# Kernel tuning notes

Hardware: AMD Instinct MI355X
Metric: run time of the kernel (lower is better)

The kernel has to match this reference:

```python
import jax, jax.numpy as jnp
import numpy as np

T, D, O, E, R = 16384, 4096, 4096, 8, 64  # tokens, in_feat, out_feat, n_adapters, max_rank


def setup_inputs() -> dict:
    key = jax.random.key(0)
    ks = jax.random.split(key, 6)
    x = jax.random.normal(ks[0], (T, D), jnp.float32)
    base_output = jax.random.normal(ks[1], (T, O), jnp.float32)
    A = jax.random.normal(ks[2], (E, D, R), jnp.float32) * 0.02  # loraA per adapter
    B = jax.random.normal(ks[3], (E, R, O), jnp.float32) * 0.02  # loraB per adapter
    scaling = jax.random.uniform(ks[4], (E,), jnp.float32, 0.5, 2.0)  # lora_alpha/rank per adapter
    adapter_ids = jax.random.randint(ks[5], (T,), 0, E, dtype=jnp.int32)  # per-token routing
    return {"x": x, "base_output": base_output, "A": A, "B": B,
            "scaling": scaling, "adapter_ids": adapter_ids}


def reference(x, base_output, A, B, scaling, adapter_ids):
    """S-LoRA batched multi-adapter forward: out = base + (x @ A_i) @ B_i * s_i,
    with adapter i routed per token. Expressed as E masked low-rank GEMMs
    (loop over the small fixed adapter set, vectorized over tokens)."""
    out = base_output
    for e in range(E):
        gate = (adapter_ids == e).astype(x.dtype) * scaling[e]  # (T,)
        h = x @ A[e]                                            # (T, R)
        out = out + (h @ B[e]) * gate[:, None]                  # (T, O)
    return out
```

## Files before the change

kernel.cpp:

```cpp
#include <hip/hip_runtime.h>

#define TT 16384
#define DD 4096
#define OO 4096
#define NE 8
#define RRK 64
#define KSPLIT 4
#define KCHUNK 1024

typedef _Float16 f16x8 __attribute__((ext_vector_type(8)));
typedef float f32x4 __attribute__((ext_vector_type(4)));

#define CNT_OFF 0
#define PERM_OFF 1024
#define AT_OFF (1u << 20)
#define BT_OFF (5u << 20)
#define HP_OFF (9u << 20)

__global__ void prep_kernel(const int* __restrict__ ids,
                            const float* __restrict__ A,
                            const float* __restrict__ B,
                            int* __restrict__ cnt,
                            int* __restrict__ perm,
                            _Float16* __restrict__ At,
                            _Float16* __restrict__ Bt) {
  const int bid = blockIdx.x, tid = threadIdx.x;
  if (bid < 64) {
    int t = bid * 256 + tid;
    int e = ids[t];
    int pos = atomicAdd(&cnt[e], 1);
    perm[e * TT + pos] = t;
    return;
  }
  __shared__ float tile[64][65];
  if (bid < 576) {
    int idx = bid - 64;
    int e = idx >> 6, kb = (idx & 63) << 6;
    #pragma unroll
    for (int i = 0; i < 16; ++i) {
      int lin = i * 256 + tid;
      int kr = lin >> 6, r = lin & 63;
      tile[kr][r] = A[((size_t)e * DD + kb + kr) * RRK + r];
    }
    __syncthreads();
    #pragma unroll
    for (int i = 0; i < 16; ++i) {
      int lin = i * 256 + tid;
      int r = lin >> 6, kk = lin & 63;
      At[((size_t)e * RRK + r) * DD + kb + kk] = (_Float16)tile[kk][r];
    }
  } else {
    int idx = bid - 576;
    int e = idx >> 6, ob = (idx & 63) << 6;
    #pragma unroll
    for (int i = 0; i < 16; ++i) {
      int lin = i * 256 + tid;
      int r = lin >> 6, o = lin & 63;
      tile[r][o] = B[((size_t)e * RRK + r) * OO + ob + o];
    }
    __syncthreads();
    #pragma unroll
    for (int i = 0; i < 16; ++i) {
      int lin = i * 256 + tid;
      int o = lin >> 6, r2 = lin & 63;
      Bt[((size_t)e * OO + ob + o) * RRK + r2] = (_Float16)tile[r2][o];
    }
  }
}

__global__ __launch_bounds__(256, 2)
void lora_stage1(const float* __restrict__ x,
                 const _Float16* __restrict__ At,
                 const int* __restrict__ cnt,
                 const int* __restrict__ perm,
                 _Float16* __restrict__ HP) {
  __shared__ _Float16 Xs[64][72];
  __shared__ _Float16 As[64][72];
  __shared__ int toks[64];
  const int tid = threadIdx.x;
  const int lane = tid & 63, w = tid >> 6;

  int tiles = 0;
  #pragma unroll
  for (int ee = 0; ee < NE; ++ee) tiles += (cnt[ee] + 63) >> 6;

  for (int wi = blockIdx.x; wi < tiles * KSPLIT; wi += gridDim.x) {
    int tile = wi >> 2, s = wi & 3;
    int e = 0, base = 0, n_e = 0;
    {
      int acc0 = 0;
      #pragma unroll
      for (int ee = 0; ee < NE; ++ee) {
        int c = cnt[ee];
        int tl = (c + 63) >> 6;
        if (tile >= acc0 && tile < acc0 + tl) { e = ee; base = acc0; n_e = c; }
        acc0 += tl;
      }
    }
    int m0 = (tile - base) << 6;
    int kbase = s * KCHUNK;

    if (tid < 64) {
      int rloc = m0 + tid;
      toks[tid] = (rloc < n_e) ? perm[e * TT + rloc] : -1;
    }
    __syncthreads();

    const int srow = tid >> 2;
    const int seg = (tid & 3) << 4;
    int tk0 = toks[srow];
    if (tk0 < 0) tk0 = toks[0];
    const float* xp = x + (size_t)tk0 * DD + seg;
    const _Float16* ap = At + ((size_t)e * RRK + srow) * DD + seg;

    f32x4 acc[4] = {};

    for (int k0 = kbase; k0 < kbase + KCHUNK; k0 += 64) {
      float4 v0 = *(const float4*)(xp + k0);
      float4 v1 = *(const float4*)(xp + k0 + 4);
      float4 v2 = *(const float4*)(xp + k0 + 8);
      float4 v3 = *(const float4*)(xp + k0 + 12);
      f16x8 xa, xb;
      xa[0] = (_Float16)v0.x; xa[1] = (_Float16)v0.y;
      xa[2] = (_Float16)v0.z; xa[3] = (_Float16)v0.w;
      xa[4] = (_Float16)v1.x; xa[5] = (_Float16)v1.y;
      xa[6] = (_Float16)v1.z; xa[7] = (_Float16)v1.w;
      xb[0] = (_Float16)v2.x; xb[1] = (_Float16)v2.y;
      xb[2] = (_Float16)v2.z; xb[3] = (_Float16)v2.w;
      xb[4] = (_Float16)v3.x; xb[5] = (_Float16)v3.y;
      xb[6] = (_Float16)v3.z; xb[7] = (_Float16)v3.w;
      *(f16x8*)&Xs[srow][seg] = xa;
      *(f16x8*)&Xs[srow][seg + 8] = xb;
      *(f16x8*)&As[srow][seg] = *(const f16x8*)(ap + k0);
      *(f16x8*)&As[srow][seg + 8] = *(const f16x8*)(ap + k0 + 8);
      __syncthreads();

      const int mr = w * 16 + (lane & 15);
      const int kq = (lane >> 4) << 3;
      #pragma unroll
      for (int ks = 0; ks < 2; ++ks) {
        f16x8 af = *(const f16x8*)&Xs[mr][ks * 32 + kq];
        #pragma unroll
        for (int nf = 0; nf < 4; ++nf) {
          f16x8 bfr = *(const f16x8*)&As[nf * 16 + (lane & 15)][ks * 32 + kq];
          acc[nf] = __builtin_amdgcn_mfma_f32_16x16x32_f16(af, bfr, acc[nf], 0, 0, 0);
        }
      }
      __syncthreads();
    }

    const int rq = (lane >> 4) << 2;
    #pragma unroll
    for (int rg = 0; rg < 4; ++rg) {
      int tk = toks[w * 16 + rq + rg];
      if (tk >= 0) {
        _Float16* hp = HP + ((size_t)s * TT + tk) * RRK + (lane & 15);
        #pragma unroll
        for (int nf = 0; nf < 4; ++nf) {
          hp[nf * 16] = (_Float16)acc[nf][rg];
        }
      }
    }
    __syncthreads();
  }
}

__global__ __launch_bounds__(256, 2)
void lora_stage2(const float* __restrict__ baseo,
                 const _Float16* __restrict__ Bt,
                 const _Float16* __restrict__ HP,
                 const float* __restrict__ scaling,
                 const int* __restrict__ cnt,
                 const int* __restrict__ perm,
                 float* __restrict__ out) {
  __shared__ _Float16 Hs[64][72];
  __shared__ _Float16 Bs[256][72];
  __shared__ int toks[64];
  const int tid = threadIdx.x;
  const int lane = tid & 63, w = tid >> 6;

  int tot = 0;
  #pragma unroll
  for (int ee = 0; ee < NE; ++ee) tot += ((cnt[ee] + 63) >> 6) << 4;

  for (int wi = blockIdx.x; wi < tot; wi += gridDim.x) {
    int e = 0, base = 0, n_e = 0;
    {
      int acc0 = 0;
      #pragma unroll
      for (int ee = 0; ee < NE; ++ee) {
        int c = cnt[ee];
        int tl = ((c + 63) >> 6) << 4;
        if (wi >= acc0 && wi < acc0 + tl) { e = ee; base = acc0; n_e = c; }
        acc0 += tl;
      }
    }
    int local = wi - base;
    int tiles_m = (n_e + 63) >> 6;
    int mt = local % tiles_m;
    int nt = local / tiles_m;
    int m0 = mt << 6, o0 = nt << 8;

    if (tid < 64) {
      int rloc = m0 + tid;
      toks[tid] = (rloc < n_e) ? perm[e * TT + rloc] : -1;
    }
    __syncthreads();

    {
      const f16x8* bp = (const f16x8*)(Bt + ((size_t)e * OO + o0 + tid) * RRK);
      #pragma unroll
      for (int j = 0; j < 8; ++j) *(f16x8*)&Bs[tid][j * 8] = bp[j];
    }
    {
      float s_e = scaling[e];
      int srow = tid >> 2, seg = (tid & 3) << 4;
      int tk = toks[srow];
      if (tk < 0) tk = toks[0];
      float sum[16];
      #pragma unroll
      for (int i = 0; i < 16; ++i) sum[i] = 0.f;
      #pragma unroll
      for (int s = 0; s < KSPLIT; ++s) {
        const f16x8* hp = (const f16x8*)(HP + ((size_t)s * TT + tk) * RRK + seg);
        f16x8 h0 = hp[0], h1 = hp[1];
        #pragma unroll
        for (int i = 0; i < 8; ++i) { sum[i] += (float)h0[i]; sum[8 + i] += (float)h1[i]; }
      }
      f16x8 o0v, o1v;
      #pragma unroll
      for (int i = 0; i < 8; ++i) { o0v[i] = (_Float16)(sum[i] * s_e); o1v[i] = (_Float16)(sum[8 + i] * s_e); }
      *(f16x8*)&Hs[srow][seg] = o0v;
      *(f16x8*)&Hs[srow][seg + 8] = o1v;
    }
    __syncthreads();

    f32x4 acc[16] = {};
    const int kq = (lane >> 4) << 3;
    const int lr = lane & 15;
    #pragma unroll
    for (int ks = 0; ks < 2; ++ks) {
      f16x8 hf = *(const f16x8*)&Hs[w * 16 + lr][ks * 32 + kq];
      #pragma unroll
      for (int of = 0; of < 16; ++of) {
        f16x8 bfr = *(const f16x8*)&Bs[of * 16 + lr][ks * 32 + kq];
        acc[of] = __builtin_amdgcn_mfma_f32_16x16x32_f16(bfr, hf, acc[of], 0, 0, 0);
      }
    }

    int tk = toks[w * 16 + lr];
    if (tk >= 0) {
      const int g4 = (lane >> 4) << 2;
      size_t rowoff = (size_t)tk * OO + o0 + g4;
      #pragma unroll
      for (int of = 0; of < 16; ++of) {
        size_t off = rowoff + of * 16;
        float4 b4 = *(const float4*)(baseo + off);
        float4 r4;
        r4.x = b4.x + acc[of][0];
        r4.y = b4.y + acc[of][1];
        r4.z = b4.z + acc[of][2];
        r4.w = b4.w + acc[of][3];
        *(float4*)(out + off) = r4;
      }
    }
    __syncthreads();
  }
}

extern "C" void kernel_launch(void* const* d_in, const int* in_sizes, int n_in,
                              void* d_out, int out_size, void* d_ws, size_t ws_size,
                              hipStream_t stream) {
  const float* x = (const float*)d_in[0];
  const float* baseo = (const float*)d_in[1];
  const float* A = (const float*)d_in[2];
  const float* B = (const float*)d_in[3];
  const float* scaling = (const float*)d_in[4];
  const int* ids = (const int*)d_in[5];
  float* out = (float*)d_out;
  char* ws = (char*)d_ws;

  int* cnt = (int*)(ws + CNT_OFF);
  int* perm = (int*)(ws + PERM_OFF);
  _Float16* At = (_Float16*)(ws + AT_OFF);
  _Float16* Bt = (_Float16*)(ws + BT_OFF);
  _Float16* HP = (_Float16*)(ws + HP_OFF);

  hipMemsetAsync(cnt, 0, NE * sizeof(int), stream);
  hipLaunchKernelGGL(prep_kernel, dim3(1088), dim3(256), 0, stream,
                     ids, A, B, cnt, perm, At, Bt);
  hipLaunchKernelGGL(lora_stage1, dim3(1056), dim3(256), 0, stream,
                     x, At, cnt, perm, HP);
  hipLaunchKernelGGL(lora_stage2, dim3(4208), dim3(256), 0, stream,
                     baseo, Bt, HP, scaling, cnt, perm, out);
}
```

Baseline: 300.4 us.

## Drop shared-memory staging, double K-split, add separate split-K reduce kernel

```diff
diff --git a/kernel.cpp b/kernel.cpp
--- a/kernel.cpp
+++ b/kernel.cpp
@@ -5,10 +5,11 @@
 #define OO 4096
 #define NE 8
 #define RRK 64
-#define KSPLIT 4
-#define KCHUNK 1024
+#define KSPLIT 8
+#define KCHUNK 512
 
 typedef _Float16 f16x8 __attribute__((ext_vector_type(8)));
+typedef _Float16 f16x4 __attribute__((ext_vector_type(4)));
 typedef float f32x4 __attribute__((ext_vector_type(4)));
 
 #define CNT_OFF 0
@@ -16,6 +17,7 @@
 #define AT_OFF (1u << 20)
 #define BT_OFF (5u << 20)
 #define HP_OFF (9u << 20)
+#define H_OFF (41u << 20)
 
 __global__ void prep_kernel(const int* __restrict__ ids,
                             const float* __restrict__ A,
@@ -68,24 +70,23 @@
   }
 }
 
-__global__ __launch_bounds__(256, 2)
+__global__ __launch_bounds__(256, 4)
 void lora_stage1(const float* __restrict__ x,
                  const _Float16* __restrict__ At,
                  const int* __restrict__ cnt,
                  const int* __restrict__ perm,
-                 _Float16* __restrict__ HP) {
-  __shared__ _Float16 Xs[64][72];
-  __shared__ _Float16 As[64][72];
-  __shared__ int toks[64];
+                 float* __restrict__ HP) {
   const int tid = threadIdx.x;
   const int lane = tid & 63, w = tid >> 6;
+  const int lr = lane & 15;
+  const int kq = (lane >> 4) << 3;
 
   int tiles = 0;
   #pragma unroll
   for (int ee = 0; ee < NE; ++ee) tiles += (cnt[ee] + 63) >> 6;
 
   for (int wi = blockIdx.x; wi < tiles * KSPLIT; wi += gridDim.x) {
-    int tile = wi >> 2, s = wi & 3;
+    int tile = wi >> 3, s = wi & 7;
     int e = 0, base = 0, n_e = 0;
     {
       int acc0 = 0;
@@ -100,84 +101,81 @@
     int m0 = (tile - base) << 6;
     int kbase = s * KCHUNK;
 
-    if (tid < 64) {
-      int rloc = m0 + tid;
-      toks[tid] = (rloc < n_e) ? perm[e * TT + rloc] : -1;
-    }
-    __syncthreads();
-
-    const int srow = tid >> 2;
-    const int seg = (tid & 3) << 4;
-    int tk0 = toks[srow];
-    if (tk0 < 0) tk0 = toks[0];
-    const float* xp = x + (size_t)tk0 * DD + seg;
-    const _Float16* ap = At + ((size_t)e * RRK + srow) * DD + seg;
+    int arow = m0 + w * 16 + lr;
+    int atok = perm[e * TT + (arow < n_e ? arow : n_e - 1)];
+    const float* xp = x + (size_t)atok * DD + kbase + kq;
+    const _Float16* ap = At + (size_t)e * RRK * DD + kbase + kq;
 
     f32x4 acc[4] = {};
 
-    for (int k0 = kbase; k0 < kbase + KCHUNK; k0 += 64) {
-      float4 v0 = *(const float4*)(xp + k0);
-      float4 v1 = *(const float4*)(xp + k0 + 4);
-      float4 v2 = *(const float4*)(xp + k0 + 8);
-      float4 v3 = *(const float4*)(xp + k0 + 12);
-      f16x8 xa, xb;
-      xa[0] = (_Float16)v0.x; xa[1] = (_Float16)v0.y;
-      xa[2] = (_Float16)v0.z; xa[3] = (_Float16)v0.w;
-      xa[4] = (_Float16)v1.x; xa[5] = (_Float16)v1.y;
-      xa[6] = (_Float16)v1.z; xa[7] = (_Float16)v1.w;
-      xb[0] = (_Float16)v2.x; xb[1] = (_Float16)v2.y;
-      xb[2] = (_Float16)v2.z; xb[3] = (_Float16)v2.w;
-      xb[4] = (_Float16)v3.x; xb[5] = (_Float16)v3.y;
-      xb[6] = (_Float16)v3.z; xb[7] = (_Float16)v3.w;
-      *(f16x8*)&Xs[srow][seg] = xa;
-      *(f16x8*)&Xs[srow][seg + 8] = xb;
-      *(f16x8*)&As[srow][seg] = *(const f16x8*)(ap + k0);
-      *(f16x8*)&As[srow][seg + 8] = *(const f16x8*)(ap + k0 + 8);
-      __syncthreads();
-
-      const int mr = w * 16 + (lane & 15);
-      const int kq = (lane >> 4) << 3;
+    for (int k0 = 0; k0 < KCHUNK; k0 += 64) {
+      f16x8 xa[2];
       #pragma unroll
       for (int ks = 0; ks < 2; ++ks) {
-        f16x8 af = *(const f16x8*)&Xs[mr][ks * 32 + kq];
+        float4 u0 = *(const float4*)(xp + k0 + ks * 32);
+        float4 u1 = *(const float4*)(xp + k0 + ks * 32 + 4);
+        f16x8 v;
+        v[0] = (_Float16)u0.x; v[1] = (_Float16)u0.y;
+        v[2] = (_Float16)u0.z; v[3] = (_Float16)u0.w;
+        v[4] = (_Float16)u1.x; v[5] = (_Float16)u1.y;
+        v[6] = (_Float16)u1.z; v[7] = (_Float16)u1.w;
+        xa[ks] = v;
+      }
+      #pragma unroll
+      for (int ks = 0; ks < 2; ++ks) {
         #pragma unroll
         for (int nf = 0; nf < 4; ++nf) {
-          f16x8 bfr = *(const f16x8*)&As[nf * 16 + (lane & 15)][ks * 32 + kq];
-          acc[nf] = __builtin_amdgcn_mfma_f32_16x16x32_f16(af, bfr, acc[nf], 0, 0, 0);
+          f16x8 bfr = *(const f16x8*)(ap + (size_t)(nf * 16 + lr) * DD + k0 + ks * 32);
+          acc[nf] = __builtin_amdgcn_mfma_f32_16x16x32_f16(xa[ks], bfr, acc[nf], 0, 0, 0);
         }
       }
-      __syncthreads();
     }
 
     const int rq = (lane >> 4) << 2;
     #pragma unroll
     for (int rg = 0; rg < 4; ++rg) {
-      int tk = toks[w * 16 + rq + rg];
-      if (tk >= 0) {
-        _Float16* hp = HP + ((size_t)s * TT + tk) * RRK + (lane & 15);
+      int row = m0 + w * 16 + rq + rg;
+      if (row < n_e) {
+        int tk = perm[e * TT + row];
+        float* hp = HP + ((size_t)s * TT + tk) * RRK + lr;
         #pragma unroll
-        for (int nf = 0; nf < 4; ++nf) {
-          hp[nf * 16] = (_Float16)acc[nf][rg];
-        }
-      }
-    }
-    __syncthreads();
-  }
-}
-
-__global__ __launch_bounds__(256, 2)
+        for (int nf = 0; nf < 4; ++nf) hp[nf * 16] = acc[nf][rg];
+      }
+    }
+  }
+}
+
+__global__ void lora_reduce(const float* __restrict__ HP,
+                            const float* __restrict__ scaling,
+                            const int* __restrict__ ids,
+                            _Float16* __restrict__ H) {
+  int i = blockIdx.x * 256 + threadIdx.x;
+  int t = i >> 4;
+  int rg = (i & 15) << 2;
+  float s = scaling[ids[t]];
+  f32x4 sum = {};
+  #pragma unroll
+  for (int sp = 0; sp < KSPLIT; ++sp) {
+    sum += *(const f32x4*)(HP + ((size_t)sp * TT + t) * RRK + rg);
+  }
+  f16x4 h;
+  #pragma unroll
+  for (int j = 0; j < 4; ++j) h[j] = (_Float16)(sum[j] * s);
+  *(f16x4*)(H + (size_t)t * RRK + rg) = h;
+}
+
+__global__ __launch_bounds__(256, 4)
 void lora_stage2(const float* __restrict__ baseo,
                  const _Float16* __restrict__ Bt,
-                 const _Float16* __restrict__ HP,
-                 const float* __restrict__ scaling,
+                 const _Float16* __restrict__ H,
                  const int* __restrict__ cnt,
                  const int* __restrict__ perm,
                  float* __restrict__ out) {
-  __shared__ _Float16 Hs[64][72];
-  __shared__ _Float16 Bs[256][72];
-  __shared__ int toks[64];
   const int tid = threadIdx.x;
   const int lane = tid & 63, w = tid >> 6;
+  const int lr = lane & 15;
+  const int kq = (lane >> 4) << 3;
+  const int g4 = (lane >> 4) << 2;
 
   int tot = 0;
   #pragma unroll
@@ -201,56 +199,29 @@
     int nt = local / tiles_m;
     int m0 = mt << 6, o0 = nt << 8;
 
-    if (tid < 64) {
-      int rloc = m0 + tid;
-      toks[tid] = (rloc < n_e) ? perm[e * TT + rloc] : -1;
-    }
-    __syncthreads();
-
-    {
-      const f16x8* bp = (const f16x8*)(Bt + ((size_t)e * OO + o0 + tid) * RRK);
-      #pragma unroll
-      for (int j = 0; j < 8; ++j) *(f16x8*)&Bs[tid][j * 8] = bp[j];
-    }
-    {
-      float s_e = scaling[e];
-      int srow = tid >> 2, seg = (tid & 3) << 4;
-      int tk = toks[srow];
-      if (tk < 0) tk = toks[0];
-      float sum[16];
-      #pragma unroll
-      for (int i = 0; i < 16; ++i) sum[i] = 0.f;
-      #pragma unroll
-      for (int s = 0; s < KSPLIT; ++s) {
-        const f16x8* hp = (const f16x8*)(HP + ((size_t)s * TT + tk) * RRK + seg);
-        f16x8 h0 = hp[0], h1 = hp[1];
-        #pragma unroll
-        for (int i = 0; i < 8; ++i) { sum[i] += (float)h0[i]; sum[8 + i] += (float)h1[i]; }
-      }
-      f16x8 o0v, o1v;
-      #pragma unroll
-      for (int i = 0; i < 8; ++i) { o0v[i] = (_Float16)(sum[i] * s_e); o1v[i] = (_Float16)(sum[8 + i] * s_e); }
-      *(f16x8*)&Hs[srow][seg] = o0v;
-      *(f16x8*)&Hs[srow][seg + 8] = o1v;
-    }
-    __syncthreads();
-
-    f32x4 acc[16] = {};
-    const int kq = (lane >> 4) << 3;
-    const int lr = lane & 15;
-    #pragma unroll
-    for (int ks = 0; ks < 2; ++ks) {
-      f16x8 hf = *(const f16x8*)&Hs[w * 16 + lr][ks * 32 + kq];
-      #pragma unroll
-      for (int of = 0; of < 16; ++of) {
-        f16x8 bfr = *(const f16x8*)&Bs[of * 16 + lr][ks * 32 + kq];
-        acc[of] = __builtin_amdgcn_mfma_f32_16x16x32_f16(bfr, hf, acc[of], 0, 0, 0);
-      }
-    }
-
-    int tk = toks[w * 16 + lr];
-    if (tk >= 0) {
-      const int g4 = (lane >> 4) << 2;
+    int row = m0 + w * 16 + lr;
+    bool valid = row < n_e;
+    int tk = perm[e * TT + (valid ? row : n_e - 1)];
+
+    const _Float16* hp = H + (size_t)tk * RRK + kq;
+    f16x8 hf0 = *(const f16x8*)(hp);
+    f16x8 hf1 = *(const f16x8*)(hp + 32);
+
+    const _Float16* bp = Bt + ((size_t)e * OO + o0 + lr) * RRK + kq;
+
+    f32x4 acc[16];
+    #pragma unroll
+    for (int of = 0; of < 16; ++of) acc[of] = (f32x4){0.f, 0.f, 0.f, 0.f};
+
+    #pragma unroll
+    for (int of = 0; of < 16; ++of) {
+      f16x8 b0 = *(const f16x8*)(bp + (size_t)of * 16 * RRK);
+      f16x8 b1 = *(const f16x8*)(bp + (size_t)of * 16 * RRK + 32);
+      acc[of] = __builtin_amdgcn_mfma_f32_16x16x32_f16(b0, hf0, acc[of], 0, 0, 0);
+      acc[of] = __builtin_amdgcn_mfma_f32_16x16x32_f16(b1, hf1, acc[of], 0, 0, 0);
+    }
+
+    if (valid) {
       size_t rowoff = (size_t)tk * OO + o0 + g4;
       #pragma unroll
       for (int of = 0; of < 16; ++of) {
@@ -264,7 +235,6 @@
         *(float4*)(out + off) = r4;
       }
     }
-    __syncthreads();
   }
 }
 
@@ -284,13 +254,16 @@
   int* perm = (int*)(ws + PERM_OFF);
   _Float16* At = (_Float16*)(ws + AT_OFF);
   _Float16* Bt = (_Float16*)(ws + BT_OFF);
-  _Float16* HP = (_Float16*)(ws + HP_OFF);
+  float* HP = (float*)(ws + HP_OFF);
+  _Float16* H = (_Float16*)(ws + H_OFF);
 
   hipMemsetAsync(cnt, 0, NE * sizeof(int), stream);
   hipLaunchKernelGGL(prep_kernel, dim3(1088), dim3(256), 0, stream,
                      ids, A, B, cnt, perm, At, Bt);
-  hipLaunchKernelGGL(lora_stage1, dim3(1056), dim3(256), 0, stream,
+  hipLaunchKernelGGL(lora_stage1, dim3(2048), dim3(256), 0, stream,
                      x, At, cnt, perm, HP);
-  hipLaunchKernelGGL(lora_stage2, dim3(4208), dim3(256), 0, stream,
-                     baseo, Bt, HP, scaling, cnt, perm, out);
-}
+  hipLaunchKernelGGL(lora_reduce, dim3(1024), dim3(256), 0, stream,
+                     HP, scaling, ids, H);
+  hipLaunchKernelGGL(lora_stage2, dim3(4096), dim3(256), 0, stream,
+                     baseo, Bt, H, cnt, perm, out);
+}
```

Result: slower. 349.8 us (+16.5%).

## Split-K reduction into own kernel; keep B fragments in registers across tiles

Applied to the files above, without the earlier changes.

```diff
diff --git a/kernel.cpp b/kernel.cpp
--- a/kernel.cpp
+++ b/kernel.cpp
@@ -9,6 +9,7 @@
 #define KCHUNK 1024
 
 typedef _Float16 f16x8 __attribute__((ext_vector_type(8)));
+typedef _Float16 f16x4 __attribute__((ext_vector_type(4)));
 typedef float f32x4 __attribute__((ext_vector_type(4)));
 
 #define CNT_OFF 0
@@ -16,6 +17,7 @@
 #define AT_OFF (1u << 20)
 #define BT_OFF (5u << 20)
 #define HP_OFF (9u << 20)
+#define H_OFF (18u << 20)
 
 __global__ void prep_kernel(const int* __restrict__ ids,
                             const float* __restrict__ A,
@@ -165,23 +167,46 @@
   }
 }
 
+__global__ void lora_reduce(const _Float16* __restrict__ HP,
+                            const float* __restrict__ scaling,
+                            const int* __restrict__ ids,
+                            _Float16* __restrict__ H) {
+  int i = blockIdx.x * 256 + threadIdx.x;
+  int t = i >> 4;
+  int rg = (i & 15) << 2;
+  float s = scaling[ids[t]];
+  float sum[4] = {0.f, 0.f, 0.f, 0.f};
+  #pragma unroll
+  for (int sp = 0; sp < KSPLIT; ++sp) {
+    f16x4 h = *(const f16x4*)(HP + ((size_t)sp * TT + t) * RRK + rg);
+    #pragma unroll
+    for (int j = 0; j < 4; ++j) sum[j] += (float)h[j];
+  }
+  f16x4 hv;
+  #pragma unroll
+  for (int j = 0; j < 4; ++j) hv[j] = (_Float16)(sum[j] * s);
+  *(f16x4*)(H + (size_t)t * RRK + rg) = hv;
+}
+
 __global__ __launch_bounds__(256, 2)
 void lora_stage2(const float* __restrict__ baseo,
                  const _Float16* __restrict__ Bt,
-                 const _Float16* __restrict__ HP,
-                 const float* __restrict__ scaling,
+                 const _Float16* __restrict__ H,
                  const int* __restrict__ cnt,
                  const int* __restrict__ perm,
                  float* __restrict__ out) {
-  __shared__ _Float16 Hs[64][72];
-  __shared__ _Float16 Bs[256][72];
-  __shared__ int toks[64];
   const int tid = threadIdx.x;
   const int lane = tid & 63, w = tid >> 6;
+  const int lr = lane & 15;
+  const int kq = (lane >> 4) << 3;
+  const int g4 = (lane >> 4) << 2;
 
   int tot = 0;
   #pragma unroll
-  for (int ee = 0; ee < NE; ++ee) tot += ((cnt[ee] + 63) >> 6) << 4;
+  for (int ee = 0; ee < NE; ++ee) {
+    int tl = (cnt[ee] + 63) >> 6;
+    tot += ((tl + 3) >> 2) << 4;
+  }
 
   for (int wi = blockIdx.x; wi < tot; wi += gridDim.x) {
     int e = 0, base = 0, n_e = 0;
@@ -190,81 +215,73 @@
       #pragma unroll
       for (int ee = 0; ee < NE; ++ee) {
         int c = cnt[ee];
-        int tl = ((c + 63) >> 6) << 4;
-        if (wi >= acc0 && wi < acc0 + tl) { e = ee; base = acc0; n_e = c; }
-        acc0 += tl;
+        int work = ((((c + 63) >> 6) + 3) >> 2) << 4;
+        if (wi >= acc0 && wi < acc0 + work) { e = ee; base = acc0; n_e = c; }
+        acc0 += work;
       }
     }
     int local = wi - base;
+    int panel = local & 15;
+    int ch = local >> 4;
+    int o0 = panel << 8;
+    int tbase = ch << 2;
     int tiles_m = (n_e + 63) >> 6;
-    int mt = local % tiles_m;
-    int nt = local / tiles_m;
-    int m0 = mt << 6, o0 = nt << 8;
-
-    if (tid < 64) {
-      int rloc = m0 + tid;
-      toks[tid] = (rloc < n_e) ? perm[e * TT + rloc] : -1;
-    }
-    __syncthreads();
-
+    int ntile = tiles_m - tbase;
+    if (ntile > 4) ntile = 4;
+
+    f16x8 bf0[16], bf1[16];
     {
-      const f16x8* bp = (const f16x8*)(Bt + ((size_t)e * OO + o0 + tid) * RRK);
-      #pragma unroll
-      for (int j = 0; j < 8; ++j) *(f16x8*)&Bs[tid][j * 8] = bp[j];
-    }
-    {
-      float s_e = scaling[e];
-      int srow = tid >> 2, seg = (tid & 3) << 4;
-      int tk = toks[srow];
-      if (tk < 0) tk = toks[0];
-      float sum[16];
-      #pragma unroll
-      for (int i = 0; i < 16; ++i) sum[i] = 0.f;
-      #pragma unroll
-      for (int s = 0; s < KSPLIT; ++s) {
-        const f16x8* hp = (const f16x8*)(HP + ((size_t)s * TT + tk) * RRK + seg);
-        f16x8 h0 = hp[0], h1 = hp[1];
+      const _Float16* bp = Bt + ((size_t)e * OO + o0 + lr) * RRK + kq;
+      #pragma unroll
+      for (int of = 0; of < 16; ++of) {
+        bf0[of] = *(const f16x8*)(bp + (size_t)of * 16 * RRK);
+        bf1[of] = *(const f16x8*)(bp + (size_t)of * 16 * RRK + 32);
+      }
+    }
+
+    const int prow = e * TT;
+    int row_c = tbase * 64 + w * 16 + lr;
+    bool v_c = row_c < n_e;
+    int tk_c = perm[prow + (v_c ? row_c : n_e - 1)];
+    f16x8 hf0_c = *(const f16x8*)(H + (size_t)tk_c * RRK + kq);
+    f16x8 hf1_c = *(const f16x8*)(H + (size_t)tk_c * RRK + kq + 32);
+
+    for (int m = 0; m < ntile; ++m) {
+      int row_n = row_c + 64;
+      bool v_n = false; int tk_n = tk_c;
+      f16x8 hf0_n = hf0_c, hf1_n = hf1_c;
+      if (m + 1 < ntile) {
+        v_n = row_n < n_e;
+        tk_n = perm[prow + (v_n ? row_n : n_e - 1)];
+        hf0_n = *(const f16x8*)(H + (size_t)tk_n * RRK + kq);
+        hf1_n = *(const f16x8*)(H + (size_t)tk_n * RRK + kq + 32);
+      }
+
+      f32x4 acc[16];
+      #pragma unroll
+      for (int of = 0; of < 16; ++of) acc[of] = (f32x4){0.f, 0.f, 0.f, 0.f};
+      #pragma unroll
+      for (int of = 0; of < 16; ++of) {
+        acc[of] = __builtin_amdgcn_mfma_f32_16x16x32_f16(bf0[of], hf0_c, acc[of], 0, 0, 0);
+        acc[of] = __builtin_amdgcn_mfma_f32_16x16x32_f16(bf1[of], hf1_c, acc[of], 0, 0, 0);
+      }
+
+      if (v_c) {
+        size_t rowoff = (size_t)tk_c * OO + o0 + g4;
         #pragma unroll
-        for (int i = 0; i < 8; ++i) { sum[i] += (float)h0[i]; sum[8 + i] += (float)h1[i]; }
-      }
-      f16x8 o0v, o1v;
-      #pragma unroll
-      for (int i = 0; i < 8; ++i) { o0v[i] = (_Float16)(sum[i] * s_e); o1v[i] = (_Float16)(sum[8 + i] * s_e); }
-      *(f16x8*)&Hs[srow][seg] = o0v;
-      *(f16x8*)&Hs[srow][seg + 8] = o1v;
-    }
-    __syncthreads();
-
-    f32x4 acc[16] = {};
-    const int kq = (lane >> 4) << 3;
-    const int lr = lane & 15;
-    #pragma unroll
-    for (int ks = 0; ks < 2; ++ks) {
-      f16x8 hf = *(const f16x8*)&Hs[w * 16 + lr][ks * 32 + kq];
-      #pragma unroll
-      for (int of = 0; of < 16; ++of) {
-        f16x8 bfr = *(const f16x8*)&Bs[of * 16 + lr][ks * 32 + kq];
-        acc[of] = __builtin_amdgcn_mfma_f32_16x16x32_f16(bfr, hf, acc[of], 0, 0, 0);
-      }
-    }
-
-    int tk = toks[w * 16 + lr];
-    if (tk >= 0) {
-      const int g4 = (lane >> 4) << 2;
-      size_t rowoff = (size_t)tk * OO + o0 + g4;
-      #pragma unroll
-      for (int of = 0; of < 16; ++of) {
-        size_t off = rowoff + of * 16;
-        float4 b4 = *(const float4*)(baseo + off);
-        float4 r4;
-        r4.x = b4.x + acc[of][0];
-        r4.y = b4.y + acc[of][1];
-        r4.z = b4.z + acc[of][2];
-        r4.w = b4.w + acc[of][3];
-        *(float4*)(out + off) = r4;
-      }
-    }
-    __syncthreads();
+        for (int of = 0; of < 16; ++of) {
+          size_t off2 = rowoff + (size_t)of * 16;
+          float4 b4 = *(const float4*)(baseo + off2);
+          float4 r4;
+          r4.x = b4.x + acc[of][0];
+          r4.y = b4.y + acc[of][1];
+          r4.z = b4.z + acc[of][2];
+          r4.w = b4.w + acc[of][3];
+          *(float4*)(out + off2) = r4;
+        }
+      }
+      row_c = row_n; v_c = v_n; tk_c = tk_n; hf0_c = hf0_n; hf1_c = hf1_n;
+    }
   }
 }
 
@@ -285,12 +302,15 @@
   _Float16* At = (_Float16*)(ws + AT_OFF);
   _Float16* Bt = (_Float16*)(ws + BT_OFF);
   _Float16* HP = (_Float16*)(ws + HP_OFF);
+  _Float16* H = (_Float16*)(ws + H_OFF);
 
   hipMemsetAsync(cnt, 0, NE * sizeof(int), stream);
   hipLaunchKernelGGL(prep_kernel, dim3(1088), dim3(256), 0, stream,
                      ids, A, B, cnt, perm, At, Bt);
   hipLaunchKernelGGL(lora_stage1, dim3(1056), dim3(256), 0, stream,
                      x, At, cnt, perm, HP);
-  hipLaunchKernelGGL(lora_stage2, dim3(4208), dim3(256), 0, stream,
-                     baseo, Bt, HP, scaling, cnt, perm, out);
-}
+  hipLaunchKernelGGL(lora_reduce, dim3(1024), dim3(256), 0, stream,
+                     HP, scaling, ids, H);
+  hipLaunchKernelGGL(lora_stage2, dim3(1024), dim3(256), 0, stream,
+                     baseo, Bt, H, cnt, perm, out);
+}
```

Result: slower. 338.4 us (+12.6%).

## Restructure LoRA stage2: register-held H, direct B loads, LDS transpose for coalesced output

Applied to the files above, without the earlier changes.

```diff
diff --git a/kernel.cpp b/kernel.cpp
--- a/kernel.cpp
+++ b/kernel.cpp
@@ -9,6 +9,7 @@
 #define KCHUNK 1024
 
 typedef _Float16 f16x8 __attribute__((ext_vector_type(8)));
+typedef _Float16 f16x4 __attribute__((ext_vector_type(4)));
 typedef float f32x4 __attribute__((ext_vector_type(4)));
 
 #define CNT_OFF 0
@@ -165,7 +166,7 @@
   }
 }
 
-__global__ __launch_bounds__(256, 2)
+__global__ __launch_bounds__(256, 4)
 void lora_stage2(const float* __restrict__ baseo,
                  const _Float16* __restrict__ Bt,
                  const _Float16* __restrict__ HP,
@@ -173,96 +174,102 @@
                  const int* __restrict__ cnt,
                  const int* __restrict__ perm,
                  float* __restrict__ out) {
-  __shared__ _Float16 Hs[64][72];
-  __shared__ _Float16 Bs[256][72];
   __shared__ int toks[64];
+  __shared__ f32x4 ldsT[2048];
   const int tid = threadIdx.x;
   const int lane = tid & 63, w = tid >> 6;
-
-  int tot = 0;
+  const int lr = lane & 15, g = lane >> 4;
+  const int kq = g << 3;
+
+  int tiles = 0;
   #pragma unroll
-  for (int ee = 0; ee < NE; ++ee) tot += ((cnt[ee] + 63) >> 6) << 4;
+  for (int ee = 0; ee < NE; ++ee) tiles += (cnt[ee] + 63) >> 6;
+  int tot = tiles << 2;
 
   for (int wi = blockIdx.x; wi < tot; wi += gridDim.x) {
-    int e = 0, base = 0, n_e = 0;
+    int tile = wi >> 2, pg = wi & 3;
+    int e = 0, m0 = 0, n_e = 0;
     {
       int acc0 = 0;
       #pragma unroll
       for (int ee = 0; ee < NE; ++ee) {
         int c = cnt[ee];
-        int tl = ((c + 63) >> 6) << 4;
-        if (wi >= acc0 && wi < acc0 + tl) { e = ee; base = acc0; n_e = c; }
+        int tl = (c + 63) >> 6;
+        if (tile >= acc0 && tile < acc0 + tl) { e = ee; m0 = (tile - acc0) << 6; n_e = c; }
         acc0 += tl;
       }
     }
-    int local = wi - base;
-    int tiles_m = (n_e + 63) >> 6;
-    int mt = local % tiles_m;
-    int nt = local / tiles_m;
-    int m0 = mt << 6, o0 = nt << 8;
-
     if (tid < 64) {
       int rloc = m0 + tid;
       toks[tid] = (rloc < n_e) ? perm[e * TT + rloc] : -1;
     }
     __syncthreads();
 
+    float s_e = scaling[e];
+    int tokA = toks[w * 16 + lr];
+    if (tokA < 0) tokA = toks[0];
+    f16x8 hf0, hf1;
     {
-      const f16x8* bp = (const f16x8*)(Bt + ((size_t)e * OO + o0 + tid) * RRK);
-      #pragma unroll
-      for (int j = 0; j < 8; ++j) *(f16x8*)&Bs[tid][j * 8] = bp[j];
-    }
-    {
-      float s_e = scaling[e];
-      int srow = tid >> 2, seg = (tid & 3) << 4;
-      int tk = toks[srow];
-      if (tk < 0) tk = toks[0];
       float sum[16];
       #pragma unroll
       for (int i = 0; i < 16; ++i) sum[i] = 0.f;
       #pragma unroll
-      for (int s = 0; s < KSPLIT; ++s) {
-        const f16x8* hp = (const f16x8*)(HP + ((size_t)s * TT + tk) * RRK + seg);
-        f16x8 h0 = hp[0], h1 = hp[1];
+      for (int sp = 0; sp < KSPLIT; ++sp) {
+        const f16x8* hp = (const f16x8*)(HP + ((size_t)sp * TT + tokA) * RRK + kq);
+        f16x8 h0 = hp[0];
+        f16x8 h1 = hp[4];
         #pragma unroll
         for (int i = 0; i < 8; ++i) { sum[i] += (float)h0[i]; sum[8 + i] += (float)h1[i]; }
       }
-      f16x8 o0v, o1v;
-      #pragma unroll
-      for (int i = 0; i < 8; ++i) { o0v[i] = (_Float16)(sum[i] * s_e); o1v[i] = (_Float16)(sum[8 + i] * s_e); }
-      *(f16x8*)&Hs[srow][seg] = o0v;
-      *(f16x8*)&Hs[srow][seg + 8] = o1v;
-    }
-    __syncthreads();
-
-    f32x4 acc[16] = {};
-    const int kq = (lane >> 4) << 3;
-    const int lr = lane & 15;
-    #pragma unroll
-    for (int ks = 0; ks < 2; ++ks) {
-      f16x8 hf = *(const f16x8*)&Hs[w * 16 + lr][ks * 32 + kq];
-      #pragma unroll
-      for (int of = 0; of < 16; ++of) {
-        f16x8 bfr = *(const f16x8*)&Bs[of * 16 + lr][ks * 32 + kq];
-        acc[of] = __builtin_amdgcn_mfma_f32_16x16x32_f16(bfr, hf, acc[of], 0, 0, 0);
-      }
-    }
-
-    int tk = toks[w * 16 + lr];
-    if (tk >= 0) {
-      const int g4 = (lane >> 4) << 2;
-      size_t rowoff = (size_t)tk * OO + o0 + g4;
-      #pragma unroll
-      for (int of = 0; of < 16; ++of) {
-        size_t off = rowoff + of * 16;
-        float4 b4 = *(const float4*)(baseo + off);
-        float4 r4;
-        r4.x = b4.x + acc[of][0];
-        r4.y = b4.y + acc[of][1];
-        r4.z = b4.z + acc[of][2];
-        r4.w = b4.w + acc[of][3];
-        *(float4*)(out + off) = r4;
-      }
+      #pragma unroll
+      for (int i = 0; i < 8; ++i) {
+        hf0[i] = (_Float16)(sum[i] * s_e);
+        hf1[i] = (_Float16)(sum[8 + i] * s_e);
+      }
+    }
+
+    const _Float16* bbase = Bt + (size_t)e * OO * RRK;
+
+    for (int ph = 0; ph < 8; ++ph) {
+      int colh = (pg << 10) + (ph << 7);
+      const _Float16* bp = bbase + (size_t)(colh + lr) * RRK + kq;
+
+      f32x4 acc[8];
+      #pragma unroll
+      for (int of = 0; of < 8; ++of) acc[of] = (f32x4){0.f, 0.f, 0.f, 0.f};
+      #pragma unroll
+      for (int of = 0; of < 8; ++of) {
+        f16x8 b0 = *(const f16x8*)(bp + (size_t)of * 16 * RRK);
+        f16x8 b1 = *(const f16x8*)(bp + (size_t)of * 16 * RRK + 32);
+        acc[of] = __builtin_amdgcn_mfma_f32_16x16x32_f16(b0, hf0, acc[of], 0, 0, 0);
+        acc[of] = __builtin_amdgcn_mfma_f32_16x16x32_f16(b1, hf1, acc[of], 0, 0, 0);
+      }
+
+      #pragma unroll
+      for (int of = 0; of < 8; ++of) {
+        int cq = (of << 2) + g;
+        ldsT[(w << 9) + (lr << 5) + (cq ^ (lr & 7))] = acc[of];
+      }
+      asm volatile("s_waitcnt lgkmcnt(0)" ::: "memory");
+      __builtin_amdgcn_sched_barrier(0);
+
+      #pragma unroll
+      for (int j = 0; j < 16; ++j) {
+        int row = m0 + (w << 4) + j;
+        if (row < n_e) {
+          int tkj = toks[(w << 4) + j];
+          int slot = (lane >> 1) ^ (j & 7);
+          const float2* lp = (const float2*)(ldsT + (w << 9) + (j << 5) + slot);
+          float2 v = lp[lane & 1];
+          size_t off = (size_t)tkj * OO + colh + (lane << 1);
+          float2 b2 = *(const float2*)(baseo + off);
+          float2 r2;
+          r2.x = b2.x + v.x;
+          r2.y = b2.y + v.y;
+          *(float2*)(out + off) = r2;
+        }
+      }
+      __builtin_amdgcn_sched_barrier(0);
     }
     __syncthreads();
   }
@@ -291,6 +298,6 @@
                      ids, A, B, cnt, perm, At, Bt);
   hipLaunchKernelGGL(lora_stage1, dim3(1056), dim3(256), 0, stream,
                      x, At, cnt, perm, HP);
-  hipLaunchKernelGGL(lora_stage2, dim3(4208), dim3(256), 0, stream,
+  hipLaunchKernelGGL(lora_stage2, dim3(1024), dim3(256), 0, stream,
                      baseo, Bt, HP, scaling, cnt, perm, out);
 }
```

Measured after the change: 417.6 us. 1.39x slower.
